# Kernel optimization log

Hardware: AMD Instinct MI355X
Metric: run time of the kernel (lower is better)

Reference implementation:

```python
import jax, jax.numpy as jnp
import numpy as np

NUM_RULES = 8192
NUM_NT = 16
RULES_PER_NT = NUM_RULES // NUM_NT  # contiguous action blocks per non-terminal
NUM_SYM = 80                        # ids 0..15 non-terminals, 16..79 terminals
EMB = 1024
HID = 1024
MAX_STEPS = 1024                    # bounded version of the data-dependent while-loop
MAX_STACK = MAX_STEPS + 4
PAD = -1                            # padding_action


def setup_inputs() -> dict:
    key = jax.random.key(0)
    ks = jax.random.split(key, 12)
    k = 1.0 / np.sqrt(HID)
    u = lambda kk, shape: jax.random.uniform(kk, shape, jnp.float32, -k, k)
    emb = jax.random.normal(ks[0], (NUM_RULES + 1, EMB), jnp.float32) * 0.02
    emb = emb.at[0].set(0.0)  # padding_idx row (action -1 + offset 1)
    inp = dict(
        emb=emb,
        Wih1=u(ks[1], (3 * HID, 2 * EMB)), Whh1=u(ks[2], (3 * HID, HID)),
        bih1=u(ks[3], (3 * HID,)), bhh1=u(ks[4], (3 * HID,)),
        Wih2=u(ks[5], (3 * HID, HID)), Whh2=u(ks[6], (3 * HID, HID)),
        bih2=u(ks[7], (3 * HID,)), bhh2=u(ks[8], (3 * HID,)),
        Wa=u(ks[9], (NUM_RULES, HID)), ba=u(ks[10], (NUM_RULES,)),
        h0=jax.random.normal(ks[11], (2, 1, HID), jnp.float32) / np.sqrt(2 * HID),
    )
    # non-terminal child -> supercritical tree, so generation runs full MAX_STEPS
    rng = np.random.RandomState(0)
    is_nt = rng.rand(NUM_RULES, 2) < 0.8
    nt_ids = rng.randint(0, NUM_NT, (NUM_RULES, 2))
    term_ids = rng.randint(NUM_NT, NUM_SYM, (NUM_RULES, 2))
    inp["children_table"] = jnp.asarray(np.where(is_nt, nt_ids, term_ids), jnp.int32)
    return inp


def _gru_cell(x, h, Wih, Whh, bih, bhh):
    gi = Wih @ x + bih
    gh = Whh @ h + bhh
    ir, iz, inn = jnp.split(gi, 3)
    hr, hz, hn = jnp.split(gh, 3)
    r = jax.nn.sigmoid(ir + hr)
    z = jax.nn.sigmoid(iz + hz)
    n = jnp.tanh(inn + r * hn)
    return (1.0 - z) * n + z * h


def reference(emb, Wih1, Whh1, bih1, bhh1, Wih2, Whh2, bih2, bhh2, Wa, ba, h0, children_table):
    kbase = jax.random.key(42)
    rule_nt = jnp.arange(NUM_RULES, dtype=jnp.int32) // RULES_PER_NT  # owning NT per action

    stack0 = jnp.full((MAX_STACK, 2), PAD, jnp.int32)
    stack0 = stack0.at[0].set(jnp.array([0, PAD], jnp.int32))  # start symbol id 0
    carry0 = (stack0, jnp.int32(1), jnp.int32(PAD), h0[:, 0, :])

    def step(carry, t):
        stack, ptr, prev_action, h = carry
        active = ptr > 0
        idx = jnp.maximum(ptr - 1, 0)
        symbol_id, parent_action = stack[idx, 0], stack[idx, 1]
        do_expand = active & (symbol_id < NUM_NT)  # terminals are popped silently
        # embedding lookup (+1 action offset), 2-layer GRU cell, action head
        x = jnp.concatenate([emb[prev_action + 1], emb[parent_action + 1]])
        h1 = _gru_cell(x, h[0], Wih1, Whh1, bih1, bhh1)
        h2 = _gru_cell(h1, h[1], Wih2, Whh2, bih2, bhh2)
        logits = Wa @ h2 + ba
        # log_softmax then mask -inf then Categorical == categorical on masked logits
        masked = jnp.where(rule_nt == symbol_id, logits, -1e9)
        action = jax.random.categorical(jax.random.fold_in(kbase, t), masked).astype(jnp.int32)
        ch = children_table[action]  # (2,) children symbol ids
        # pop one, push reversed(children): child[1] lower, child[0] on top
        j1 = jnp.minimum(idx + 1, MAX_STACK - 1)
        row0 = jnp.where(do_expand, jnp.stack([ch[1], action]), stack[idx])
        row1 = jnp.where(do_expand, jnp.stack([ch[0], action]), stack[j1])
        stack = stack.at[idx].set(row0).at[j1].set(row1)
        ptr = jnp.where(do_expand, jnp.minimum(idx + 2, MAX_STACK),
                        jnp.where(active, ptr - 1, ptr)).astype(jnp.int32)
        prev_action = jnp.where(do_expand, action, prev_action)
        h = jnp.where(do_expand, jnp.stack([h1, h2]), h)
        out_action = jnp.where(do_expand, action, jnp.int32(PAD))
        return (stack, ptr, prev_action, h), out_action

    (_, _, _, h_fin), actions = jax.lax.scan(step, carry0, jnp.arange(MAX_STEPS))
    return actions, h_fin[:, None, :]
```

## Files before the change

### kernel.cpp

```cpp
#include <hip/hip_runtime.h>
#include <stdint.h>


#define NBLK   256
#define NTHR   256
#define HID_   1024
#define RPB    12
#define NSTEP  1024
#define STK    1028
#define NUMNT  16
#define JAX_PARTITIONABLE 1

__device__ __forceinline__ uint32_t rotl32(uint32_t v, int d){ return (v<<d)|(v>>(32-d)); }

__device__ __forceinline__ void tf2x32(uint32_t k0, uint32_t k1, uint32_t x0, uint32_t x1,
                                       uint32_t& o0, uint32_t& o1){
  uint32_t k2 = k0 ^ k1 ^ 0x1BD11BDAu;
  x0 += k0; x1 += k1;
  x0+=x1; x1=rotl32(x1,13); x1^=x0;
  x0+=x1; x1=rotl32(x1,15); x1^=x0;
  x0+=x1; x1=rotl32(x1,26); x1^=x0;
  x0+=x1; x1=rotl32(x1, 6); x1^=x0;
  x0+=k1; x1+=k2+1u;
  x0+=x1; x1=rotl32(x1,17); x1^=x0;
  x0+=x1; x1=rotl32(x1,29); x1^=x0;
  x0+=x1; x1=rotl32(x1,16); x1^=x0;
  x0+=x1; x1=rotl32(x1,24); x1^=x0;
  x0+=k2; x1+=k0+2u;
  x0+=x1; x1=rotl32(x1,13); x1^=x0;
  x0+=x1; x1=rotl32(x1,15); x1^=x0;
  x0+=x1; x1=rotl32(x1,26); x1^=x0;
  x0+=x1; x1=rotl32(x1, 6); x1^=x0;
  x0+=k0; x1+=k1+3u;
  x0+=x1; x1=rotl32(x1,17); x1^=x0;
  x0+=x1; x1=rotl32(x1,29); x1^=x0;
  x0+=x1; x1=rotl32(x1,16); x1^=x0;
  x0+=x1; x1=rotl32(x1,24); x1^=x0;
  x0+=k1; x1+=k2+4u;
  x0+=x1; x1=rotl32(x1,13); x1^=x0;
  x0+=x1; x1=rotl32(x1,15); x1^=x0;
  x0+=x1; x1=rotl32(x1,26); x1^=x0;
  x0+=x1; x1=rotl32(x1, 6); x1^=x0;
  x0+=k2; x1+=k0+5u;
  o0 = x0; o1 = x1;
}

__device__ __forceinline__ float gumbel_at(int t, int q){
  uint32_t fk0, fk1, a, c, bits;
  tf2x32(0u, 42u, 0u, (uint32_t)t, fk0, fk1);
#if JAX_PARTITIONABLE
  tf2x32(fk0, fk1, 0u, (uint32_t)q, a, c);
  bits = a ^ c;
#else
  if (q < 4096){ tf2x32(fk0, fk1, (uint32_t)q, (uint32_t)(q+4096), a, c); bits = a; }
  else         { tf2x32(fk0, fk1, (uint32_t)(q-4096), (uint32_t)q, a, c); bits = c; }
#endif
  float f = __uint_as_float((bits >> 9) | 0x3f800000u) - 1.0f;
  float u = fmaxf(1.17549435e-38f, f);
  return -logf(-logf(u));
}

__device__ __forceinline__ float sigf(float x){ return 0.5f + 0.5f * tanhf(0.5f * x); }

__device__ __forceinline__ float gload(const float* p){
  return __hip_atomic_load(p, __ATOMIC_RELAXED, __HIP_MEMORY_SCOPE_AGENT);
}
__device__ __forceinline__ float2 gload2(const float* p){
  union { unsigned long long u; float2 f; } v;
  v.u = __hip_atomic_load((const unsigned long long*)p, __ATOMIC_RELAXED,
                          __HIP_MEMORY_SCOPE_AGENT);
  return v.f;
}
__device__ __forceinline__ void gstore(float* p, float v){
  __hip_atomic_store(p, v, __ATOMIC_RELAXED, __HIP_MEMORY_SCOPE_AGENT);
}

__global__ __launch_bounds__(NTHR, 1)
void tree_gen(const float* __restrict__ emb,  const float* __restrict__ Wih1,
              const float* __restrict__ Whh1, const float* __restrict__ bih1,
              const float* __restrict__ bhh1, const float* __restrict__ Wih2,
              const float* __restrict__ Whh2, const float* __restrict__ bih2,
              const float* __restrict__ bhh2, const float* __restrict__ Wa,
              const float* __restrict__ ba,   const float* __restrict__ h0,
              const int* __restrict__ ctab,
              float* __restrict__ out,
              float* __restrict__ h1g, float* __restrict__ h2g,
              unsigned long long* __restrict__ winner,
              unsigned* __restrict__ gcnt, unsigned* __restrict__ root,
              unsigned* __restrict__ flag)
{
  __shared__ __align__(16) float sWhh1[RPB*HID_];
  __shared__ __align__(16) float sWih2[RPB*HID_];
  __shared__ __align__(16) float sWhh2[RPB*HID_];
  __shared__ __align__(16) float sH[HID_];
  __shared__ short sSym[STK];
  __shared__ short sAct[STK];
  __shared__ float sGh1[RPB], sGh2[RPB], sGi[RPB];
  __shared__ float sBih1[RPB], sBih2[RPB], sBhh1[RPB], sBhh2[RPB];
  __shared__ float sH1o[4], sH2o[4];
  __shared__ float sLV[2];
  __shared__ int   sPtr, sPrev;
  __shared__ int   sDead;

  const int tid  = threadIdx.x;
  const int b    = blockIdx.x;
  const int wid  = tid >> 6;
  const int lane = tid & 63;
  unsigned ep = 0;
  int eix = 0;

  auto gbar = [&](unsigned epoch){
    __syncthreads();
    if (tid == 0 && !sDead){
      asm volatile("s_waitcnt vmcnt(0)" ::: "memory");
      unsigned* gc = gcnt + ((b >> 3) << 4);
      unsigned o = __hip_atomic_fetch_add(gc, 1u, __ATOMIC_RELAXED, __HIP_MEMORY_SCOPE_AGENT);
      if (o == (epoch << 3) - 1u){
        unsigned r = __hip_atomic_fetch_add(root, 1u, __ATOMIC_RELAXED, __HIP_MEMORY_SCOPE_AGENT);
        if (r == (epoch << 5) - 1u)
          __hip_atomic_store(flag, epoch, __ATOMIC_RELAXED, __HIP_MEMORY_SCOPE_AGENT);
      }
      unsigned tries = 0;
      while (__hip_atomic_load(flag, __ATOMIC_RELAXED, __HIP_MEMORY_SCOPE_AGENT) < epoch){
        __builtin_amdgcn_s_sleep(2);
        if (++tries > 2000000u){ sDead = 1; break; }
      }
    }
    __syncthreads();
  };

  for (int j = 0; j < RPB; ++j){
    const int r = (j >> 2) * HID_ + (b << 2) + (j & 3);
    const float* a1 = Whh1 + (size_t)r * HID_;
    const float* a2 = Wih2 + (size_t)r * HID_;
    const float* a3 = Whh2 + (size_t)r * HID_;
    for (int c = tid * 4; c < HID_; c += NTHR * 4){
      *(float4*)&sWhh1[j*HID_ + c] = *(const float4*)(a1 + c);
      *(float4*)&sWih2[j*HID_ + c] = *(const float4*)(a2 + c);
      *(float4*)&sWhh2[j*HID_ + c] = *(const float4*)(a3 + c);
    }
  }
  if (tid < RPB){
    const int r = (tid >> 2) * HID_ + (b << 2) + (tid & 3);
    sBih1[tid] = bih1[r]; sBih2[tid] = bih2[r];
    sBhh1[tid] = bhh1[r]; sBhh2[tid] = bhh2[r];
  }
  if (tid == 0){ sSym[0] = 0; sAct[0] = -1; sPtr = 1; sPrev = -1; sDead = 0; }
  if (tid < 4){
    float v1 = h0[(b<<2)+tid];
    float v2 = h0[HID_+(b<<2)+tid];
    sH1o[tid] = v1; sH2o[tid] = v2;
    gstore(h1g + (b<<2)+tid, v1);
    gstore(h2g + (b<<2)+tid, v2);
  }

  float4 wA[3][8];
  #pragma unroll
  for (int jj = 0; jj < 3; ++jj){
    const int j = wid + 4*jj;
    const int r = (j >> 2) * HID_ + (b << 2) + (j & 3);
    const float* wr = Wih1 + (size_t)r * 2048 + 4*lane;
    #pragma unroll
    for (int it = 0; it < 4; ++it){
      wA[jj][it]     = *(const float4*)(wr + 256*it);
      wA[jj][4 + it] = *(const float4*)(wr + 1024 + 256*it);
    }
  }
  __syncthreads();

  {
    float4 x1[4], x2[4];
    #pragma unroll
    for (int it=0; it<4; ++it){
      x1[it] = *(const float4*)(h0 + 4*lane + 256*it);
      x2[it] = *(const float4*)(h0 + HID_ + 4*lane + 256*it);
    }
    #pragma unroll
    for (int jj=0; jj<3; ++jj){
      const int j = wid + 4*jj;
      float a1 = 0.f, a2 = 0.f;
      #pragma unroll
      for (int it=0; it<4; ++it){
        float4 w1 = *(const float4*)&sWhh1[j*HID_ + 4*lane + 256*it];
        float4 w2 = *(const float4*)&sWhh2[j*HID_ + 4*lane + 256*it];
        a1 += w1.x*x1[it].x + w1.y*x1[it].y + w1.z*x1[it].z + w1.w*x1[it].w;
        a2 += w2.x*x2[it].x + w2.y*x2[it].y + w2.z*x2[it].z + w2.w*x2[it].w;
      }
      #pragma unroll
      for (int m=32; m; m>>=1){ a1 += __shfl_xor(a1, m); a2 += __shfl_xor(a2, m); }
      if (lane == 0){ sGh1[j] = a1 + sBhh1[j]; sGh2[j] = a2 + sBhh2[j]; }
    }
  }
  __syncthreads();

  for (int t = 0; t < NSTEP; ++t){
    const int  ptr    = sPtr;
    const bool active = ptr > 0;
    const int  idx    = active ? (ptr - 1) : 0;
    const int  sym    = sSym[idx];
    const int  parent = sAct[idx];
    const int  prev   = sPrev;
    const bool expand = active && (sym < NUMNT);

    if (!expand){
      __syncthreads();
      if (tid == 0){
        if (active) sPtr = ptr - 1;
        if (b == 0) out[t] = -1.0f;
      }
      __syncthreads();
      continue;
    }

    {
      const float* embP = emb + (size_t)(prev + 1) * HID_ + 4*lane;
      const float* embQ = emb + (size_t)(parent + 1) * HID_ + 4*lane;
      float4 xp[4], xq[4];
      #pragma unroll
      for (int it=0; it<4; ++it){
        xp[it] = *(const float4*)(embP + 256*it);
        xq[it] = *(const float4*)(embQ + 256*it);
      }
      #pragma unroll
      for (int jj=0; jj<3; ++jj){
        float acc = 0.f;
        #pragma unroll
        for (int it=0; it<4; ++it){
          acc += wA[jj][it].x*xp[it].x + wA[jj][it].y*xp[it].y
               + wA[jj][it].z*xp[it].z + wA[jj][it].w*xp[it].w;
        }
        #pragma unroll
        for (int it=0; it<4; ++it){
          acc += wA[jj][4+it].x*xq[it].x + wA[jj][4+it].y*xq[it].y
               + wA[jj][4+it].z*xq[it].z + wA[jj][4+it].w*xq[it].w;
        }
        #pragma unroll
        for (int m=32; m; m>>=1) acc += __shfl_xor(acc, m);
        if (lane == 0) sGi[wid + 4*jj] = acc + sBih1[wid + 4*jj];
      }
      __syncthreads();
      if (tid < 4){
        float rr = sigf(sGi[tid]    + sGh1[tid]);
        float zz = sigf(sGi[4+tid]  + sGh1[4+tid]);
        float nn = tanhf(sGi[8+tid] + rr * sGh1[8+tid]);
        float nh = (1.f - zz)*nn + zz*sH1o[tid];
        sH1o[tid] = nh;
        gstore(h1g + (b<<2)+tid, nh);
      }
    }
    gbar(++ep);

    {
      if (b == 0 && tid == 0)
        __hip_atomic_store(winner + ((eix + 2) & 3), 0ull,
                           __ATOMIC_RELAXED, __HIP_MEMORY_SCOPE_AGENT);
      {
        const int c = tid << 2;
        float2 lo = gload2(h1g + c);
        float2 hi = gload2(h1g + c + 2);
        *(float4*)&sH[c] = make_float4(lo.x, lo.y, hi.x, hi.y);
      }
      __syncthreads();
      #pragma unroll
      for (int jj=0; jj<3; ++jj){
        const int j = wid + 4*jj;
        float ai = 0.f, ah = 0.f;
        #pragma unroll
        for (int it=0; it<4; ++it){
          float4 xr = *(const float4*)&sH[4*lane + 256*it];
          float4 w2 = *(const float4*)&sWih2[j*HID_ + 4*lane + 256*it];
          float4 w1 = *(const float4*)&sWhh1[j*HID_ + 4*lane + 256*it];
          ai += w2.x*xr.x + w2.y*xr.y + w2.z*xr.z + w2.w*xr.w;
          ah += w1.x*xr.x + w1.y*xr.y + w1.z*xr.z + w1.w*xr.w;
        }
        #pragma unroll
        for (int m=32; m; m>>=1){ ai += __shfl_xor(ai, m); ah += __shfl_xor(ah, m); }
        if (lane == 0){ sGi[j] = ai + sBih2[j]; sGh1[j] = ah + sBhh1[j]; }
      }
      __syncthreads();
      if (tid < 4){
        float rr = sigf(sGi[tid]    + sGh2[tid]);
        float zz = sigf(sGi[4+tid]  + sGh2[4+tid]);
        float nn = tanhf(sGi[8+tid] + rr * sGh2[8+tid]);
        float nh = (1.f - zz)*nn + zz*sH2o[tid];
        sH2o[tid] = nh;
        gstore(h2g + (b<<2)+tid, nh);
      }
    }
    gbar(++ep);

    {
      {
        const int c = tid << 2;
        float2 lo = gload2(h2g + c);
        float2 hi = gload2(h2g + c + 2);
        *(float4*)&sH[c] = make_float4(lo.x, lo.y, hi.x, hi.y);
      }
      __syncthreads();
      #pragma unroll
      for (int jj=0; jj<3; ++jj){
        const int j = wid + 4*jj;
        float ah = 0.f;
        #pragma unroll
        for (int it=0; it<4; ++it){
          float4 xr = *(const float4*)&sH[4*lane + 256*it];
          float4 w  = *(const float4*)&sWhh2[j*HID_ + 4*lane + 256*it];
          ah += w.x*xr.x + w.y*xr.y + w.z*xr.z + w.w*xr.w;
        }
        #pragma unroll
        for (int m=32; m; m>>=1) ah += __shfl_xor(ah, m);
        if (lane == 0) sGh2[j] = ah + sBhh2[j];
      }
      if (wid < 2){
        const int q = sym*512 + (b<<1) + wid;
        const float* wr = Wa + (size_t)q * HID_ + 4*lane;
        float acc = 0.f;
        #pragma unroll
        for (int it=0; it<4; ++it){
          float4 xr = *(const float4*)&sH[4*lane + 256*it];
          float4 w  = *(const float4*)(wr + 256*it);
          acc += w.x*xr.x + w.y*xr.y + w.z*xr.z + w.w*xr.w;
        }
        #pragma unroll
        for (int m=32; m; m>>=1) acc += __shfl_xor(acc, m);
        if (lane == 0) sLV[wid] = acc + ba[q] + gumbel_at(t, q);
      }
      __syncthreads();
      if (tid == 0){
        const int q0 = sym*512 + (b<<1);
        float v; int q;
        if (sLV[1] > sLV[0]){ v = sLV[1]; q = q0 + 1; }
        else                { v = sLV[0]; q = q0;     }
        unsigned ub   = __float_as_uint(v);
        unsigned mono = (ub & 0x80000000u) ? ~ub : (ub | 0x80000000u);
        unsigned long long key = ((unsigned long long)mono << 13)
                               | (unsigned long long)(8191 - q);
        __hip_atomic_fetch_max(winner + (eix & 3), key,
                               __ATOMIC_RELAXED, __HIP_MEMORY_SCOPE_AGENT);
      }
    }
    gbar(++ep);

    if (tid == 0){
      unsigned long long w = __hip_atomic_load(winner + (eix & 3), __ATOMIC_RELAXED,
                                               __HIP_MEMORY_SCOPE_AGENT);
      const int action = 8191 - (int)(w & 8191ull);
      const int ch0 = ctab[2*action];
      const int ch1 = ctab[2*action + 1];
      sSym[idx] = (short)ch1; sAct[idx] = (short)action;
      int j1 = idx + 1; if (j1 > STK-1) j1 = STK-1;
      sSym[j1] = (short)ch0; sAct[j1] = (short)action;
      int np = idx + 2; if (np > STK) np = STK;
      sPtr = np; sPrev = action;
      if (b == 0) out[t] = (float)action;
    }
    __syncthreads();
    ++eix;
  }

  if (b == 0){
    for (int i = tid; i < HID_; i += NTHR){
      out[NSTEP + i]        = gload(h1g + i);
      out[NSTEP + HID_ + i] = gload(h2g + i);
    }
  }
}

extern "C" void kernel_launch(void* const* d_in, const int* in_sizes, int n_in,
                              void* d_out, int out_size, void* d_ws, size_t ws_size,
                              hipStream_t stream) {
  (void)in_sizes; (void)n_in; (void)out_size; (void)ws_size;
  const float* emb  = (const float*)d_in[0];
  const float* Wih1 = (const float*)d_in[1];
  const float* Whh1 = (const float*)d_in[2];
  const float* bih1 = (const float*)d_in[3];
  const float* bhh1 = (const float*)d_in[4];
  const float* Wih2 = (const float*)d_in[5];
  const float* Whh2 = (const float*)d_in[6];
  const float* bih2 = (const float*)d_in[7];
  const float* bhh2 = (const float*)d_in[8];
  const float* Wa   = (const float*)d_in[9];
  const float* ba   = (const float*)d_in[10];
  const float* h0   = (const float*)d_in[11];
  const int*   ctab = (const int*)d_in[12];
  float* out = (float*)d_out;

  char* ws = (char*)d_ws;
  unsigned* gcnt = (unsigned*)ws;
  unsigned* root = (unsigned*)(ws + 2048);
  unsigned* flag = (unsigned*)(ws + 2112);
  unsigned long long* winner = (unsigned long long*)(ws + 2176);
  float* h1g = (float*)(ws + 4096);
  float* h2g = (float*)(ws + 8192);

  hipMemsetAsync(d_ws, 0, 4096, stream);
  tree_gen<<<NBLK, NTHR, 0, stream>>>(emb, Wih1, Whh1, bih1, bhh1, Wih2, Whh2,
                                      bih2, bhh2, Wa, ba, h0, ctab, out,
                                      h1g, h2g, winner, gcnt, root, flag);
}
```

Baseline: 18.27 ms.

## Use XCC-aware hierarchical grid barrier and prefetch Wa rows early

Replaces the fixed two-level block-index grid barrier with one organised by hardware XCC ID. Blocks on the same XCC arrive on a per-XCC counter using workgroup-scope atomics, and one leader per XCC exchanges with the other XCCs, so most polling stays inside the XCC's L2. An init rendezvous first counts how many blocks landed on each XCC. Separately, the Wa row, bias and gumbel noise are loaded before the GRU compute so their latency is hidden. The risk is that workgroup-scope atomics on global memory may not be coherent across CUs within an XCC, and the scheme adds an initial barrier.

```diff
diff --git a/kernel.cpp b/kernel.cpp
--- a/kernel.cpp
+++ b/kernel.cpp
@@ -74,6 +74,12 @@
 __device__ __forceinline__ void gstore(float* p, float v){
   __hip_atomic_store(p, v, __ATOMIC_RELAXED, __HIP_MEMORY_SCOPE_AGENT);
 }
+__device__ __forceinline__ unsigned lpoll(unsigned* p){
+  unsigned e = 0xFFFFFFFFu;
+  __hip_atomic_compare_exchange_strong(p, &e, 0xFFFFFFFFu,
+      __ATOMIC_RELAXED, __ATOMIC_RELAXED, __HIP_MEMORY_SCOPE_WORKGROUP);
+  return e;
+}
 
 __global__ __launch_bounds__(NTHR, 1)
 void tree_gen(const float* __restrict__ emb,  const float* __restrict__ Wih1,
@@ -86,8 +92,7 @@
               float* __restrict__ out,
               float* __restrict__ h1g, float* __restrict__ h2g,
               unsigned long long* __restrict__ winner,
-              unsigned* __restrict__ gcnt, unsigned* __restrict__ root,
-              unsigned* __restrict__ flag)
+              unsigned* __restrict__ ctrl)
 {
   __shared__ __align__(16) float sWhh1[RPB*HID_];
   __shared__ __align__(16) float sWih2[RPB*HID_];
@@ -109,21 +114,55 @@
   unsigned ep = 0;
   int eix = 0;
 
+  unsigned xcc;
+  asm volatile("s_getreg_b32 %0, hwreg(HW_REG_XCC_ID)" : "=s"(xcc));
+  xcc &= 7u;
+  unsigned* leaf     = ctrl + xcc*32;
+  unsigned* lfl      = ctrl + 256 + xcc*32;
+  unsigned* arr8     = ctrl + 512;
+  unsigned* xcdCount = ctrl + 544;
+  unsigned* initCnt  = ctrl + 576;
+  unsigned* initFlag = ctrl + 608;
+  unsigned myCnt = 0;
+
+  if (tid == 0){
+    sSym[0] = 0; sAct[0] = -1; sPtr = 1; sPrev = -1; sDead = 0;
+    __hip_atomic_fetch_add(&xcdCount[xcc], 1u, __ATOMIC_RELAXED, __HIP_MEMORY_SCOPE_AGENT);
+    asm volatile("s_waitcnt vmcnt(0)" ::: "memory");
+    unsigned o = __hip_atomic_fetch_add(initCnt, 1u, __ATOMIC_RELAXED, __HIP_MEMORY_SCOPE_AGENT);
+    if (o == NBLK - 1u)
+      __hip_atomic_store(initFlag, 1u, __ATOMIC_RELAXED, __HIP_MEMORY_SCOPE_AGENT);
+    unsigned tries = 0;
+    while (__hip_atomic_load(initFlag, __ATOMIC_RELAXED, __HIP_MEMORY_SCOPE_AGENT) < 1u){
+      __builtin_amdgcn_s_sleep(2);
+      if (++tries > 2000000u){ sDead = 1; break; }
+    }
+    myCnt = __hip_atomic_load(&xcdCount[xcc], __ATOMIC_RELAXED, __HIP_MEMORY_SCOPE_AGENT);
+  }
+
   auto gbar = [&](unsigned epoch){
     __syncthreads();
     if (tid == 0 && !sDead){
       asm volatile("s_waitcnt vmcnt(0)" ::: "memory");
-      unsigned* gc = gcnt + ((b >> 3) << 4);
-      unsigned o = __hip_atomic_fetch_add(gc, 1u, __ATOMIC_RELAXED, __HIP_MEMORY_SCOPE_AGENT);
-      if (o == (epoch << 3) - 1u){
-        unsigned r = __hip_atomic_fetch_add(root, 1u, __ATOMIC_RELAXED, __HIP_MEMORY_SCOPE_AGENT);
-        if (r == (epoch << 5) - 1u)
-          __hip_atomic_store(flag, epoch, __ATOMIC_RELAXED, __HIP_MEMORY_SCOPE_AGENT);
-      }
-      unsigned tries = 0;
-      while (__hip_atomic_load(flag, __ATOMIC_RELAXED, __HIP_MEMORY_SCOPE_AGENT) < epoch){
-        __builtin_amdgcn_s_sleep(2);
-        if (++tries > 2000000u){ sDead = 1; break; }
+      unsigned o = __hip_atomic_fetch_add(leaf, 1u, __ATOMIC_RELAXED,
+                                          __HIP_MEMORY_SCOPE_WORKGROUP);
+      if (o == myCnt * epoch - 1u){
+        __hip_atomic_store(&arr8[xcc], epoch, __ATOMIC_RELAXED, __HIP_MEMORY_SCOPE_AGENT);
+        unsigned tries = 0;
+        for (int x = 0; x < 8; ){
+          unsigned v = __hip_atomic_load(&arr8[x], __ATOMIC_RELAXED, __HIP_MEMORY_SCOPE_AGENT);
+          if (v >= epoch){ ++x; continue; }
+          __builtin_amdgcn_s_sleep(1);
+          if (++tries > 2000000u){ sDead = 1; break; }
+        }
+        __hip_atomic_store(lfl, epoch, __ATOMIC_RELAXED, __HIP_MEMORY_SCOPE_WORKGROUP);
+        asm volatile("s_waitcnt vmcnt(0)" ::: "memory");
+      } else {
+        unsigned tries = 0;
+        while (lpoll(lfl) < epoch){
+          __builtin_amdgcn_s_sleep(1);
+          if (++tries > 4000000u){ sDead = 1; break; }
+        }
       }
     }
     __syncthreads();
@@ -145,7 +184,6 @@
     sBih1[tid] = bih1[r]; sBih2[tid] = bih2[r];
     sBhh1[tid] = bhh1[r]; sBhh2[tid] = bhh2[r];
   }
-  if (tid == 0){ sSym[0] = 0; sAct[0] = -1; sPtr = 1; sPrev = -1; sDead = 0; }
   if (tid < 4){
     float v1 = h0[(b<<2)+tid];
     float v2 = h0[HID_+(b<<2)+tid];
@@ -212,6 +250,16 @@
       continue;
     }
 
+    float4 wv[4]; float bq = 0.f, gmb = 0.f; int q = 0;
+    if (wid < 2){
+      q = sym*512 + (b<<1) + wid;
+      const float* wr = Wa + (size_t)q * HID_ + 4*lane;
+      #pragma unroll
+      for (int it=0; it<4; ++it) wv[it] = *(const float4*)(wr + 256*it);
+      bq  = ba[q];
+      gmb = gumbel_at(t, q);
+    }
+
     {
       const float* embP = emb + (size_t)(prev + 1) * HID_ + 4*lane;
       const float* embQ = emb + (size_t)(parent + 1) * HID_ + 4*lane;
@@ -312,29 +360,26 @@
         if (lane == 0) sGh2[j] = ah + sBhh2[j];
       }
       if (wid < 2){
-        const int q = sym*512 + (b<<1) + wid;
-        const float* wr = Wa + (size_t)q * HID_ + 4*lane;
         float acc = 0.f;
         #pragma unroll
         for (int it=0; it<4; ++it){
           float4 xr = *(const float4*)&sH[4*lane + 256*it];
-          float4 w  = *(const float4*)(wr + 256*it);
-          acc += w.x*xr.x + w.y*xr.y + w.z*xr.z + w.w*xr.w;
+          acc += wv[it].x*xr.x + wv[it].y*xr.y + wv[it].z*xr.z + wv[it].w*xr.w;
         }
         #pragma unroll
         for (int m=32; m; m>>=1) acc += __shfl_xor(acc, m);
-        if (lane == 0) sLV[wid] = acc + ba[q] + gumbel_at(t, q);
+        if (lane == 0) sLV[wid] = acc + bq + gmb;
       }
       __syncthreads();
       if (tid == 0){
         const int q0 = sym*512 + (b<<1);
-        float v; int q;
-        if (sLV[1] > sLV[0]){ v = sLV[1]; q = q0 + 1; }
-        else                { v = sLV[0]; q = q0;     }
+        float v; int qq;
+        if (sLV[1] > sLV[0]){ v = sLV[1]; qq = q0 + 1; }
+        else                { v = sLV[0]; qq = q0;     }
         unsigned ub   = __float_as_uint(v);
         unsigned mono = (ub & 0x80000000u) ? ~ub : (ub | 0x80000000u);
         unsigned long long key = ((unsigned long long)mono << 13)
-                               | (unsigned long long)(8191 - q);
+                               | (unsigned long long)(8191 - qq);
         __hip_atomic_fetch_max(winner + (eix & 3), key,
                                __ATOMIC_RELAXED, __HIP_MEMORY_SCOPE_AGENT);
       }
@@ -386,15 +431,13 @@
   float* out = (float*)d_out;
 
   char* ws = (char*)d_ws;
-  unsigned* gcnt = (unsigned*)ws;
-  unsigned* root = (unsigned*)(ws + 2048);
-  unsigned* flag = (unsigned*)(ws + 2112);
-  unsigned long long* winner = (unsigned long long*)(ws + 2176);
+  unsigned* ctrl = (unsigned*)ws;
+  unsigned long long* winner = (unsigned long long*)(ws + 3072);
   float* h1g = (float*)(ws + 4096);
   float* h2g = (float*)(ws + 8192);
 
   hipMemsetAsync(d_ws, 0, 4096, stream);
   tree_gen<<<NBLK, NTHR, 0, stream>>>(emb, Wih1, Whh1, bih1, bhh1, Wih2, Whh2,
                                       bih2, bhh2, Wa, ba, h0, ctab, out,
-                                      h1g, h2g, winner, gcnt, root, flag);
-}
+                                      h1g, h2g, winner, ctrl);
+}
```

New measurement: 14.63 ms. 19.9% less time.
